# Kernel tuning notes

Hardware: AMD Instinct MI355X
Metric: run time of the kernel (lower is better)

## Reference

```python
import jax, jax.numpy as jnp
import numpy as np

N_NODES = 100000
N_EDGES = 1600000
NFEAT = 128
NHID = 64
N_CLUSTERS = 20
ALPHA = 0.2


def setup_inputs() -> dict:
    key = jax.random.key(0)
    ks = jax.random.split(key, 6)
    stdv = 1.0 / np.sqrt(NHID)
    x = jax.random.normal(ks[0], (N_NODES, NFEAT), dtype=jnp.float32)
    edge_index = jax.random.randint(ks[1], (2, N_EDGES), 0, N_NODES, dtype=jnp.int64)
    edge_weight = jax.random.uniform(ks[2], (N_EDGES,), dtype=jnp.float32)
    W = jax.random.uniform(ks[3], (NFEAT, NHID), minval=-stdv, maxval=stdv, dtype=jnp.float32)
    b = jax.random.uniform(ks[4], (NHID,), minval=-stdv, maxval=stdv, dtype=jnp.float32)
    mu = jax.random.normal(ks[5], (N_CLUSTERS, NHID), dtype=jnp.float32)
    return {"x": x, "edge_index": edge_index, "edge_weight": edge_weight,
            "W": W, "b": b, "mu": mu}


def _gcn_conv(x, edge_index, edge_weight, W, b):
    # PyG GCNConv: add self loops (weight 1), symmetric normalization,
    # out[i] = sum_j norm_ij * (x[j] @ W) + b
    N = x.shape[0]
    loop = jnp.arange(N, dtype=edge_index.dtype)
    src = jnp.concatenate([edge_index[0], loop])
    dst = jnp.concatenate([edge_index[1], loop])
    w = jnp.concatenate([edge_weight, jnp.ones((N,), dtype=x.dtype)])
    deg = jax.ops.segment_sum(w, dst, num_segments=N)  # [N]
    dinv = jnp.where(deg > 0, jax.lax.rsqrt(deg), 0.0)
    norm = dinv[src] * w * dinv[dst]                   # [E+N]
    support = x @ W                                    # [N, nhid]
    msgs = support[src] * norm[:, None]                # [E+N, nhid] gather
    out = jax.ops.segment_sum(msgs, dst, num_segments=N)  # scatter-add
    return out + b


def reference(x, edge_index, edge_weight, W, b, mu):
    z = _gcn_conv(x, edge_index, edge_weight, W, b)    # [N, nhid]
    # Student-t soft assignment (DEC head)
    d2 = jnp.sum((z[:, None, :] - mu[None, :, :]) ** 2, axis=2)  # [N, K]
    q = 1.0 / (1.0 + d2 / ALPHA + 1e-8)
    q = q ** (ALPHA + 1.0) / 2.0
    q = q / jnp.sum(q, axis=1, keepdims=True)
    return (z, q)
```

## Files before the change

### kernel.cpp

```cpp
#include <hip/hip_runtime.h>

#define NN 100000
#define NE 1600000
#define NF 128
#define NH 64
#define NK 20
#define SBK 512
#define NSB ((NN + SBK - 1) / SBK)
#define CAP 9216
#define CT 4096
#define PAD 8
#define MAXPAIRS (size_t(NE) + size_t(PAD) * NN)

static constexpr float ALPHA = 0.2f;

typedef unsigned short u16;
typedef unsigned int u32;

constexpr size_t alup(size_t x) { return (x + 255) & ~size_t(255); }
constexpr size_t O_FLAG   = 0;
constexpr size_t O_GCNT   = 64;
constexpr size_t O_DINV   = 256;
constexpr size_t O_HIST   = alup(O_DINV + size_t(NN) * 4);
constexpr size_t O_OFF    = alup(O_HIST + size_t(NN) * 4);
constexpr size_t O_BCUR   = alup(O_OFF  + size_t(NN) * 4);
constexpr size_t O_COARSE = alup(O_BCUR + size_t(NSB) * 4);
constexpr size_t O_EPAIR  = alup(O_COARSE + size_t(NSB) * CAP * 8);
constexpr size_t O_SUP    = alup(O_EPAIR + MAXPAIRS * 8);

__device__ __forceinline__ u16 f2bf(float f) {
  u32 u = __float_as_uint(f);
  u32 r = (u + 0x7fffu + ((u >> 16) & 1u)) >> 16;
  return (u16)r;
}

__global__ __launch_bounds__(256) void k_detect(const void* ei, int* flag, int* bcur, int* gcnt) {
  __shared__ int bad;
  if (threadIdx.x == 0) { bad = 0; *gcnt = 0; }
  if (threadIdx.x < NSB) bcur[threadIdx.x] = threadIdx.x * CAP;
  __syncthreads();
  const long long* p = (const long long*)ei;
  int ok = 1;
#pragma unroll
  for (int k = 0; k < 4; ++k) {
    long long v = p[threadIdx.x * 4 + k];
    if (v < 0 || v >= NN) ok = 0;
  }
  if (!ok) atomicOr(&bad, 1);
  __syncthreads();
  if (threadIdx.x == 0) *flag = bad ? 0 : 1;
}

__global__ __launch_bounds__(256) void k_coarse(const void* ei, const int* __restrict__ flag,
                                                const float* __restrict__ w,
                                                int* bcur, uint2* __restrict__ coarse) {
  __shared__ int lh[NSB];
  __shared__ int lbase[NSB];
  int t = threadIdx.x;
  for (int i = t; i < NSB; i += 256) lh[i] = 0;
  __syncthreads();
  int base = blockIdx.x * CT;
  int is64 = *flag;
  u32 key[16]; int wb[16], bk[16], lr[16];
#pragma unroll
  for (int k = 0; k < 16; ++k) {
    int e = base + k * 256 + t;
    if (e < NE) {
      int s, d;
      if (is64) { const long long* p = (const long long*)ei; s = (int)p[e]; d = (int)p[NE + e]; }
      else      { const int*       p = (const int*)ei;       s = p[e];      d = p[NE + e]; }
      int bb = d >> 9, dlo = d & 511;
      key[k] = (u32)s | ((u32)dlo << 17);
      wb[k]  = __float_as_int(w[e]);
      bk[k]  = bb;
      lr[k]  = atomicAdd(&lh[bb], 1);
    }
  }
  __syncthreads();
  if (t < NSB) { int c = lh[t]; if (c) lbase[t] = atomicAdd(&bcur[t], c); }
  __syncthreads();
#pragma unroll
  for (int k = 0; k < 16; ++k) {
    int e = base + k * 256 + t;
    if (e < NE) coarse[lbase[bk[k]] + lr[k]] = make_uint2(key[k], (u32)wb[k]);
  }
}

__global__ __launch_bounds__(256) void k_sort(const uint2* __restrict__ coarse,
                                              const int* __restrict__ bcur,
                                              int* __restrict__ gcnt,
                                              int* __restrict__ hist,
                                              float* __restrict__ dinv,
                                              int* __restrict__ off,
                                              int2* __restrict__ epair) {
  __shared__ int cnt[SBK];
  __shared__ float wsum[SBK];
  __shared__ int cur[SBK];
  __shared__ int endi[SBK];
  __shared__ int wtot[4];
  __shared__ int gbase;
  int t = threadIdx.x, b = blockIdx.x;
  for (int i = t; i < SBK; i += 256) { cnt[i] = 0; wsum[i] = 0.f; }
  __syncthreads();
  int s = b * CAP, e = bcur[b];
  for (int j = s + t; j < e; j += 256) {
    uint2 u = coarse[j];
    int dlo = u.x >> 17;
    atomicAdd(&cnt[dlo], 1);
    atomicAdd(&wsum[dlo], __uint_as_float(u.y));
  }
  __syncthreads();
  int n0 = b * SBK + t * 2, n1 = n0 + 1;
  int c0r = cnt[t * 2], c1r = cnt[t * 2 + 1];
  int c0 = (c0r + (PAD - 1)) & ~(PAD - 1);
  int c1 = (c1r + (PAD - 1)) & ~(PAD - 1);
  int sum2 = c0 + c1;
  int lane = t & 63, wv = t >> 6;
  int inc = sum2;
  for (int d = 1; d < 64; d <<= 1) { int tt = __shfl_up(inc, d, 64); if (lane >= d) inc += tt; }
  if (lane == 63) wtot[wv] = inc;
  __syncthreads();
  if (t == 0) gbase = atomicAdd(gcnt, wtot[0] + wtot[1] + wtot[2] + wtot[3]);
  int wbase = 0;
#pragma unroll
  for (int k = 0; k < 4; ++k) if (k < wv) wbase += wtot[k];
  __syncthreads();
  int base0 = gbase + wbase + (inc - sum2);
  int base1 = base0 + c0;
  if (n0 < NN) { off[n0] = base0; hist[n0] = c0r; dinv[n0] = rsqrtf(1.0f + wsum[t * 2]); }
  if (n1 < NN) { off[n1] = base1; hist[n1] = c1r; dinv[n1] = rsqrtf(1.0f + wsum[t * 2 + 1]); }
  cur[t * 2]      = base0;
  cur[t * 2 + 1]  = base1;
  endi[t * 2]     = base0 + c0;
  endi[t * 2 + 1] = base1 + c1;
  __syncthreads();
  for (int j = s + t; j < e; j += 256) {
    uint2 u = coarse[j];
    int dlo = u.x >> 17;
    int src = u.x & 0x1FFFF;
    int pos = atomicAdd(&cur[dlo], 1);
    epair[pos] = make_int2(src, (int)u.y);
  }
  __syncthreads();
#pragma unroll
  for (int h = 0; h < 2; ++h) {
    int i = t * 2 + h;
    for (int p = cur[i]; p < endi[i]; ++p) epair[p] = make_int2(0, 0);
  }
}

__global__ __launch_bounds__(256) void k_gemm(const float* __restrict__ x,
                                              const float* __restrict__ W,
                                              const float* __restrict__ dinv,
                                              u16* __restrict__ supb) {
  __shared__ float4 Wl[NF * NH / 4];
  const float4* Wg = (const float4*)W;
  for (int i = threadIdx.x; i < NF * NH / 4; i += 256) Wl[i] = Wg[i];
  __syncthreads();
  int lane16 = threadIdx.x & 15;
  int rowin  = threadIdx.x >> 4;
  const float4* x4 = (const float4*)x;
  int rowbase = blockIdx.x * 128;
  for (int r0 = 0; r0 < 128; r0 += 16) {
    int r = rowbase + r0 + rowin;
    if (r >= NN) return;
    float4 acc = make_float4(0.f, 0.f, 0.f, 0.f);
#pragma unroll 8
    for (int kk = 0; kk < NF / 4; ++kk) {
      float4 xv = x4[r * (NF / 4) + kk];
      float4 w0 = Wl[(4 * kk + 0) * 16 + lane16];
      float4 w1 = Wl[(4 * kk + 1) * 16 + lane16];
      float4 w2 = Wl[(4 * kk + 2) * 16 + lane16];
      float4 w3 = Wl[(4 * kk + 3) * 16 + lane16];
      acc.x += xv.x * w0.x + xv.y * w1.x + xv.z * w2.x + xv.w * w3.x;
      acc.y += xv.x * w0.y + xv.y * w1.y + xv.z * w2.y + xv.w * w3.y;
      acc.z += xv.x * w0.z + xv.y * w1.z + xv.z * w2.z + xv.w * w3.z;
      acc.w += xv.x * w0.w + xv.y * w1.w + xv.z * w2.w + xv.w * w3.w;
    }
    float di = dinv[r];
    ushort4 o;
    o.x = f2bf(acc.x * di); o.y = f2bf(acc.y * di);
    o.z = f2bf(acc.z * di); o.w = f2bf(acc.w * di);
    *(ushort4*)&supb[(size_t)r * NH + lane16 * 4] = o;
  }
}

__global__ __launch_bounds__(256) void k_agg_q(const int2* __restrict__ epair,
                                               const int* __restrict__ off,
                                               const int* __restrict__ hist,
                                               const float* __restrict__ dinv,
                                               const u16* __restrict__ supb,
                                               const float* __restrict__ b,
                                               const float* __restrict__ mu,
                                               float* __restrict__ z,
                                               float* __restrict__ q) {
  __shared__ float muL[NK * 68];
  __shared__ float zsh[4][64];
  for (int i = threadIdx.x; i < NK * NH; i += 256) muL[(i >> 6) * 68 + (i & 63)] = mu[i];
  __syncthreads();
  int wid  = (blockIdx.x * 256 + threadIdx.x) >> 6;
  int lane = threadIdx.x & 63;
  int wv   = threadIdx.x >> 6;

  int startU = __builtin_amdgcn_readfirstlane(off[wid]);
  int cntU   = __builtin_amdgcn_readfirstlane(hist[wid]);
  int endU   = startU + ((cntU + (PAD - 1)) & ~(PAD - 1));
  float di   = dinv[wid];
  int  hi    = lane >> 5;
  u32  loff  = ((u32)(lane & 31)) << 2;

  u32 su = *(const u32*)((const char*)supb + (((u32)wid) << 7) + loff);
  float aLo = hi ? 0.f : __uint_as_float(su << 16);
  float aHi = hi ? 0.f : __uint_as_float(su & 0xffff0000u);

  for (int j = startU; j < endU; j += 8) {
    int4 p01 = *(const int4*)&epair[j + 0];
    int4 p23 = *(const int4*)&epair[j + 2];
    int4 p45 = *(const int4*)&epair[j + 4];
    int4 p67 = *(const int4*)&epair[j + 6];
#pragma unroll
    for (int k = 0; k < 4; ++k) {
      int4 p = (k == 0) ? p01 : (k == 1) ? p23 : (k == 2) ? p45 : p67;
      int   src = hi ? p.z : p.x;
      float wgt = __int_as_float(hi ? p.w : p.y);
      u32 u = *(const u32*)((const char*)supb + (((u32)src) << 7) + loff);
      aLo += wgt * __uint_as_float(u << 16);
      aHi += wgt * __uint_as_float(u & 0xffff0000u);
    }
  }
  aLo += __shfl_xor(aLo, 32, 64);
  aHi += __shfl_xor(aHi, 32, 64);

  int fp = lane & 31;
  float2 bb = *(const float2*)&b[fp * 2];
  float zLo = di * aLo + bb.x;
  float zHi = di * aHi + bb.y;
  if (hi == 0) {
    *(float2*)&z[(size_t)wid * NH + fp * 2] = make_float2(zLo, zHi);
    *(float2*)&zsh[wv][fp * 2] = make_float2(zLo, zHi);
  }

  float qv = 0.f;
  if (lane < NK) {
    const float4* zr = (const float4*)zsh[wv];
    const float4* mr = (const float4*)&muL[lane * 68];
    float s0 = 0.f, s1 = 0.f, s2 = 0.f, s3 = 0.f;
#pragma unroll
    for (int j = 0; j < 16; ++j) {
      float4 zv = zr[j];
      float4 mv = mr[j];
      float a0 = zv.x - mv.x, a1 = zv.y - mv.y, a2 = zv.z - mv.z, a3 = zv.w - mv.w;
      s0 += a0 * a0; s1 += a1 * a1; s2 += a2 * a2; s3 += a3 * a3;
    }
    float d2 = (s0 + s1) + (s2 + s3);
    float tq = 1.0f / (1.0f + d2 * (1.0f / ALPHA) + 1e-8f);
    qv = exp2f((ALPHA + 1.0f) * __log2f(tq));
  }
  float ssum = qv;
  for (int o = 32; o; o >>= 1) ssum += __shfl_xor(ssum, o, 64);
  if (lane < NK) q[(size_t)wid * NK + lane] = qv / ssum;
}

extern "C" void kernel_launch(void* const* d_in, const int* in_sizes, int n_in,
                              void* d_out, int out_size, void* d_ws, size_t ws_size,
                              hipStream_t stream) {
  const float* x  = (const float*)d_in[0];
  const void*  ei = d_in[1];
  const float* w  = (const float*)d_in[2];
  const float* W  = (const float*)d_in[3];
  const float* b  = (const float*)d_in[4];
  const float* mu = (const float*)d_in[5];

  char* ws = (char*)d_ws;
  int*   flag   = (int*)(ws + O_FLAG);
  int*   gcnt   = (int*)(ws + O_GCNT);
  float* dinv   = (float*)(ws + O_DINV);
  int*   hist   = (int*)(ws + O_HIST);
  int*   off    = (int*)(ws + O_OFF);
  int*   bcur   = (int*)(ws + O_BCUR);
  uint2* coarse = (uint2*)(ws + O_COARSE);
  int2*  epair  = (int2*)(ws + O_EPAIR);
  u16*   supb   = (u16*)(ws + O_SUP);

  float* z = (float*)d_out;
  float* q = (float*)d_out + (size_t)NN * NH;

  hipLaunchKernelGGL(k_detect, dim3(1),                   dim3(256), 0, stream, ei, flag, bcur, gcnt);
  hipLaunchKernelGGL(k_coarse, dim3((NE + CT - 1) / CT),  dim3(256), 0, stream, ei, flag, w, bcur, coarse);
  hipLaunchKernelGGL(k_sort,   dim3(NSB),                 dim3(256), 0, stream, coarse, bcur, gcnt, hist, dinv, off, epair);
  hipLaunchKernelGGL(k_gemm,   dim3((NN + 127) / 128),    dim3(256), 0, stream, x, W, dinv, supb);
  hipLaunchKernelGGL(k_agg_q,  dim3((NN * 64) / 256),     dim3(256), 0, stream, epair, off, hist, dinv, supb, b, mu, z, q);
}
```

Baseline: 177.1 us.

## Gather one bf16 feature per lane and split distance computation across wave halves

The aggregation loop previously used half-waves, each lane loading a packed pair of bf16 features for one of two edges at a time. Now every lane loads a single 2-byte bf16 feature per edge, handling all eight edges per step with two accumulators, which removes the cross-half shuffle and the packed unpacking. The Student-t distance computation is split so both wave halves each sum 32 dimensions and then combine with a shuffle. This gives 64-lane coalesced 128-byte rows per gather but doubles the number of gather instructions per edge, and 2-byte loads may be less efficient.

```diff
diff --git a/kernel.cpp b/kernel.cpp
--- a/kernel.cpp
+++ b/kernel.cpp
@@ -32,6 +32,12 @@
   u32 u = __float_as_uint(f);
   u32 r = (u + 0x7fffu + ((u >> 16) & 1u)) >> 16;
   return (u16)r;
+}
+__device__ __forceinline__ float bf2f(u16 h) {
+  return __uint_as_float(((u32)h) << 16);
+}
+__device__ __forceinline__ float gath(const u16* supb, u32 byteoff) {
+  return bf2f(*(const u16*)((const char*)supb + byteoff));
 }
 
 __global__ __launch_bounds__(256) void k_detect(const void* ei, int* flag, int* bcur, int* gcnt) {
@@ -205,55 +211,60 @@
   int startU = __builtin_amdgcn_readfirstlane(off[wid]);
   int cntU   = __builtin_amdgcn_readfirstlane(hist[wid]);
   int endU   = startU + ((cntU + (PAD - 1)) & ~(PAD - 1));
-  float di   = dinv[wid];
-  int  hi    = lane >> 5;
-  u32  loff  = ((u32)(lane & 31)) << 2;
-
-  u32 su = *(const u32*)((const char*)supb + (((u32)wid) << 7) + loff);
-  float aLo = hi ? 0.f : __uint_as_float(su << 16);
-  float aHi = hi ? 0.f : __uint_as_float(su & 0xffff0000u);
+  float di  = dinv[wid];
+  u32 loff = (u32)lane << 1;
+  float acc0 = gath(supb, ((u32)wid << 7) + loff);
+  float acc1 = 0.f;
 
   for (int j = startU; j < endU; j += 8) {
     int4 p01 = *(const int4*)&epair[j + 0];
     int4 p23 = *(const int4*)&epair[j + 2];
     int4 p45 = *(const int4*)&epair[j + 4];
     int4 p67 = *(const int4*)&epair[j + 6];
-#pragma unroll
-    for (int k = 0; k < 4; ++k) {
-      int4 p = (k == 0) ? p01 : (k == 1) ? p23 : (k == 2) ? p45 : p67;
-      int   src = hi ? p.z : p.x;
-      float wgt = __int_as_float(hi ? p.w : p.y);
-      u32 u = *(const u32*)((const char*)supb + (((u32)src) << 7) + loff);
-      aLo += wgt * __uint_as_float(u << 16);
-      aHi += wgt * __uint_as_float(u & 0xffff0000u);
-    }
-  }
-  aLo += __shfl_xor(aLo, 32, 64);
-  aHi += __shfl_xor(aHi, 32, 64);
-
-  int fp = lane & 31;
-  float2 bb = *(const float2*)&b[fp * 2];
-  float zLo = di * aLo + bb.x;
-  float zHi = di * aHi + bb.y;
-  if (hi == 0) {
-    *(float2*)&z[(size_t)wid * NH + fp * 2] = make_float2(zLo, zHi);
-    *(float2*)&zsh[wv][fp * 2] = make_float2(zLo, zHi);
-  }
-
-  float qv = 0.f;
-  if (lane < NK) {
-    const float4* zr = (const float4*)zsh[wv];
-    const float4* mr = (const float4*)&muL[lane * 68];
-    float s0 = 0.f, s1 = 0.f, s2 = 0.f, s3 = 0.f;
-#pragma unroll
-    for (int j = 0; j < 16; ++j) {
+    float v0 = gath(supb, ((u32)p01.x << 7) + loff);
+    float v1 = gath(supb, ((u32)p01.z << 7) + loff);
+    float v2 = gath(supb, ((u32)p23.x << 7) + loff);
+    float v3 = gath(supb, ((u32)p23.z << 7) + loff);
+    float v4 = gath(supb, ((u32)p45.x << 7) + loff);
+    float v5 = gath(supb, ((u32)p45.z << 7) + loff);
+    float v6 = gath(supb, ((u32)p67.x << 7) + loff);
+    float v7 = gath(supb, ((u32)p67.z << 7) + loff);
+    acc0 += __int_as_float(p01.y) * v0;
+    acc1 += __int_as_float(p01.w) * v1;
+    acc0 += __int_as_float(p23.y) * v2;
+    acc1 += __int_as_float(p23.w) * v3;
+    acc0 += __int_as_float(p45.y) * v4;
+    acc1 += __int_as_float(p45.w) * v5;
+    acc0 += __int_as_float(p67.y) * v6;
+    acc1 += __int_as_float(p67.w) * v7;
+  }
+
+  float zz = di * (acc0 + acc1) + b[lane];
+  z[(size_t)wid * NH + lane] = zz;
+  zsh[wv][lane] = zz;
+
+  int kk = lane & 31;
+  int h  = lane >> 5;
+  float s = 0.f;
+  if (kk < NK) {
+    const float4* zr = (const float4*)&zsh[wv][h * 32];
+    const float4* mr = (const float4*)&muL[kk * 68 + h * 32];
+    float s0 = 0.f, s1 = 0.f;
+#pragma unroll
+    for (int j = 0; j < 8; ++j) {
       float4 zv = zr[j];
       float4 mv = mr[j];
       float a0 = zv.x - mv.x, a1 = zv.y - mv.y, a2 = zv.z - mv.z, a3 = zv.w - mv.w;
-      s0 += a0 * a0; s1 += a1 * a1; s2 += a2 * a2; s3 += a3 * a3;
+      s0 += a0 * a0 + a1 * a1;
+      s1 += a2 * a2 + a3 * a3;
     }
-    float d2 = (s0 + s1) + (s2 + s3);
-    float tq = 1.0f / (1.0f + d2 * (1.0f / ALPHA) + 1e-8f);
+    s = s0 + s1;
+  }
+  s += __shfl_xor(s, 32, 64);
+
+  float qv = 0.f;
+  if (lane < NK) {
+    float tq = 1.0f / (1.0f + s * (1.0f / ALPHA) + 1e-8f);
     qv = exp2f((ALPHA + 1.0f) * __log2f(tq));
   }
   float ssum = qv;
```

New measurement: 167.6 us. 5.4% less time.
